# Kernel tuning notes

Hardware: AMD Instinct MI355X
Metric: run time of the kernel (lower is better)

The kernel has to match this reference:

```python
import jax, jax.numpy as jnp
import numpy as np
from jax import lax

DIM = 192
HEADS = 4
EPS = 1e-12  # torch F.normalize eps


def setup_inputs() -> dict:
    key = jax.random.key(0)
    k1, k2, k3, k4 = jax.random.split(key, 4)
    b, c, h, w = 8, DIM, 128, 128
    x = jax.random.normal(k1, (b, c, h, w), dtype=jnp.float32)
    w_qkv = jax.random.normal(k2, (3 * c, c), dtype=jnp.float32) * (1.0 / np.sqrt(c))
    w_dw = jax.random.normal(k3, (3 * c, 1, 3, 3), dtype=jnp.float32) * (1.0 / 3.0)
    temperature = jnp.ones((HEADS, 1, 1), dtype=jnp.float32)
    w_proj = jax.random.normal(k4, (c, c), dtype=jnp.float32) * (1.0 / np.sqrt(c))
    return {"x": x, "w_qkv": w_qkv, "w_dw": w_dw, "temperature": temperature, "w_proj": w_proj}


def _l2norm(t):
    # torch F.normalize(dim=-1): t / max(||t||_2, eps)
    n = jnp.sqrt(jnp.sum(t * t, axis=-1, keepdims=True))
    return t / jnp.maximum(n, EPS)


def reference(x, w_qkv, w_dw, temperature, w_proj):
    b, c, h, w = x.shape
    heads = HEADS
    hc = c // heads  # channels per head
    # 1x1 conv: dim -> 3*dim
    qkv = jnp.einsum('bchw,oc->bohw', x, w_qkv)
    # depthwise 3x3 conv, padding=1, no relu/norm
    qkv = lax.conv_general_dilated(
        qkv, w_dw, window_strides=(1, 1), padding='SAME',
        feature_group_count=3 * c,
        dimension_numbers=('NCHW', 'OIHW', 'NCHW'))
    q, k, v = jnp.split(qkv, 3, axis=1)
    # b (head c) h w -> b head c (h w)
    n = h * w
    q = q.reshape(b, heads, hc, n)
    k = k.reshape(b, heads, hc, n)
    v = v.reshape(b, heads, hc, n)
    q = _l2norm(q)
    k = _l2norm(k)
    # channel attention: [b, head, hc, hc]
    attn = jnp.einsum('bhcn,bhdn->bhcd', q, k) * temperature[None]
    attn = jax.nn.softmax(attn, axis=-1)
    out = jnp.einsum('bhcd,bhdn->bhcn', attn, v)
    out = out.reshape(b, c, h, w)
    out = jnp.einsum('bchw,oc->bohw', out, w_proj)
    return out
```

## Files before the change

kernel.cpp:

```cpp
#include <hip/hip_runtime.h>
#include <stdint.h>


typedef __attribute__((ext_vector_type(8))) short bf16x8;
typedef __attribute__((ext_vector_type(4))) float f32x4;
typedef unsigned short u16;

#define HW 16384
#define CD 192
#define O3 576
#define KD 192

__device__ __forceinline__ float b2f(u16 u) {
    union { unsigned int i; float f; } v; v.i = ((unsigned int)u) << 16; return v.f;
}
__device__ __forceinline__ u16 f2b(float f) {
    union { float f; unsigned int i; } v; v.f = f;
    return (u16)((v.i + 0x7fffu + ((v.i >> 16) & 1u)) >> 16);
}

__global__ __launch_bounds__(256) void fill_f32(float* p, long long n, float val) {
    long long stride = (long long)gridDim.x * 256;
    for (long long i = blockIdx.x * 256LL + threadIdx.x; i < n; i += stride) p[i] = val;
}

__global__ __launch_bounds__(256) void zerof(float* p, int n) {
    int i = blockIdx.x * 256 + threadIdx.x;
    if (i < n) p[i] = 0.f;
}

__global__ __launch_bounds__(256) void cvt_f2b(const float* __restrict__ in,
                                               u16* __restrict__ out, int n) {
    int i = blockIdx.x * 256 + threadIdx.x;
    if (i < n) out[i] = f2b(in[i]);
}

__global__ __launch_bounds__(256) void transpose_f2b(
    const float* __restrict__ in, u16* __restrict__ out,
    long long in_bs, long long out_bs)
{
    __shared__ u16 t[64 * 72];
    const int tid = threadIdx.x;
    const int p0 = blockIdx.x * 64, c0 = blockIdx.y * 64;
    const long long bz = blockIdx.z;
    const float* ib = in + bz * in_bs;
    u16* ob = out + bz * out_bs;
    {
        int cl = tid >> 2, pc = (tid & 3) * 16;
        const float* src = &ib[(long long)(c0 + cl) * HW + p0 + pc];
#pragma unroll
        for (int j4 = 0; j4 < 4; j4++) {
            f32x4 v = *(const f32x4*)(src + j4 * 4);
            u16* d = &t[cl * 72 + pc + j4 * 4];
            d[0] = f2b(v[0]); d[1] = f2b(v[1]); d[2] = f2b(v[2]); d[3] = f2b(v[3]);
        }
    }
    __syncthreads();
    {
        int pl = tid >> 2, cc = (tid & 3) * 16;
        u16 tmp[16] __attribute__((aligned(16)));
#pragma unroll
        for (int j = 0; j < 16; j++) tmp[j] = t[(cc + j) * 72 + pl];
        u16* dst = &ob[(long long)(p0 + pl) * CD + c0 + cc];
        *(bf16x8*)dst       = *(const bf16x8*)&tmp[0];
        *(bf16x8*)(dst + 8) = *(const bf16x8*)&tmp[8];
    }
}

__global__ __launch_bounds__(256) void transpose_b(
    const u16* __restrict__ in, u16* __restrict__ out,
    long long in_bs, long long out_bs)
{
    __shared__ u16 t[64 * 72];
    const int tid = threadIdx.x;
    const int p0 = blockIdx.x * 64, c0 = blockIdx.y * 64;
    const long long bz = blockIdx.z;
    const u16* ib = in + bz * in_bs;
    u16* ob = out + bz * out_bs;
    {
        int cl = tid >> 2, pc = (tid & 3) * 16;
        const u16* src = &ib[(long long)(c0 + cl) * HW + p0 + pc];
        *(bf16x8*)&t[cl * 72 + pc]     = *(const bf16x8*)src;
        *(bf16x8*)&t[cl * 72 + pc + 8] = *(const bf16x8*)(src + 8);
    }
    __syncthreads();
    {
        int pl = tid >> 2, cc = (tid & 3) * 16;
        u16 tmp[16] __attribute__((aligned(16)));
#pragma unroll
        for (int j = 0; j < 16; j++) tmp[j] = t[(cc + j) * 72 + pl];
        u16* dst = &ob[(long long)(p0 + pl) * CD + c0 + cc];
        *(bf16x8*)dst       = *(const bf16x8*)&tmp[0];
        *(bf16x8*)(dst + 8) = *(const bf16x8*)&tmp[8];
    }
}

__device__ __forceinline__ void stage16(const u16* g, u16* l) {
    __builtin_amdgcn_global_load_lds((const __attribute__((address_space(1))) unsigned int*)g,
                                     (__attribute__((address_space(3))) unsigned int*)l, 16, 0, 0);
}

template <bool OUT_F32>
__global__ __launch_bounds__(256) void gemm_bt(
    const u16* __restrict__ A, const u16* __restrict__ Bt, void* __restrict__ Cv,
    int M, long long a_bs, long long b_bs, long long c_bs)
{
    __shared__ u16 lsA[128 * 32];
    __shared__ u16 lsB[128 * 32];
    const int tid = threadIdx.x;
    const int lane = tid & 63, wid = tid >> 6;
    const int n0 = blockIdx.x * 128, m0 = blockIdx.y * 128;
    const long long bz = blockIdx.z;
    const u16* Ab = A + bz * a_bs;
    const u16* Bb = Bt + bz * b_bs;
    const int wm = (wid & 1) * 64, wn = (wid >> 1) * 64;
    const int lr = lane & 15, quad = lane >> 4;
    const int srow = lane >> 2, skc = (lane & 3) * 8;

    f32x4 acc[4][4];
#pragma unroll
    for (int i = 0; i < 4; i++)
#pragma unroll
        for (int j = 0; j < 4; j++) acc[i][j] = (f32x4){0.f, 0.f, 0.f, 0.f};

    for (int k0 = 0; k0 < KD; k0 += 32) {
        __syncthreads();
#pragma unroll
        for (int i = 0; i < 2; i++) {
            int ra = m0 + wid * 32 + i * 16 + srow;
            ra = ra < M ? ra : M - 1;
            stage16(Ab + (long long)ra * KD + k0 + skc, &lsA[(wid * 32 + i * 16) * 32]);
            int rb = n0 + wid * 32 + i * 16 + srow;
            stage16(Bb + (long long)rb * KD + k0 + skc, &lsB[(wid * 32 + i * 16) * 32]);
        }
        __syncthreads();
        bf16x8 af[4], bfv[4];
#pragma unroll
        for (int t = 0; t < 4; t++) {
            af[t]  = *(const bf16x8*)&lsA[(wm + t * 16 + lr) * 32 + quad * 8];
            bfv[t] = *(const bf16x8*)&lsB[(wn + t * 16 + lr) * 32 + quad * 8];
        }
#pragma unroll
        for (int mt = 0; mt < 4; mt++)
#pragma unroll
            for (int nt = 0; nt < 4; nt++)
                acc[mt][nt] = __builtin_amdgcn_mfma_f32_16x16x32_bf16(af[mt], bfv[nt], acc[mt][nt], 0, 0, 0);
    }
#pragma unroll
    for (int mt = 0; mt < 4; mt++)
#pragma unroll
        for (int r = 0; r < 4; r++) {
            int row = m0 + wm + mt * 16 + quad * 4 + r;
            if (row < M) {
#pragma unroll
                for (int nt = 0; nt < 4; nt++) {
                    int col = n0 + wn + nt * 16 + lr;
                    if (OUT_F32)
                        ((float*)Cv)[bz * c_bs + (long long)row * HW + col] = acc[mt][nt][r];
                    else
                        ((u16*)Cv)[bz * c_bs + (long long)row * HW + col] = f2b(acc[mt][nt][r]);
                }
            }
        }
}

__global__ __launch_bounds__(256) void dwconv2(
    const u16* __restrict__ in, const float* __restrict__ wdw, u16* __restrict__ outp,
    long long in_bs, long long out_bs, int wch0)
{
    const int rt = blockIdx.x, ch = blockIdx.y, tid = threadIdx.x;
    const long long bz = blockIdx.z;
    const u16* ip = in + bz * in_bs + (long long)ch * HW;
    u16* op = outp + bz * out_bs + (long long)ch * HW;
    __shared__ float t[18 * 132];
    const int r0 = rt * 16;
    if (tid < 18) {
        t[tid * 132 + 0] = 0.f;   t[tid * 132 + 129] = 0.f;
        t[tid * 132 + 130] = 0.f; t[tid * 132 + 131] = 0.f;
    }
    for (int i = tid; i < 288; i += 256) {
        int rr = i >> 4, cc = (i & 15) * 8;
        int gr = r0 + rr - 1;
        float f[8];
        if (gr >= 0 && gr < 128) {
            bf16x8 v = *(const bf16x8*)(ip + gr * 128 + cc);
#pragma unroll
            for (int j = 0; j < 8; j++) f[j] = b2f((u16)v[j]);
        } else {
#pragma unroll
            for (int j = 0; j < 8; j++) f[j] = 0.f;
        }
#pragma unroll
        for (int j = 0; j < 8; j++) t[rr * 132 + 1 + cc + j] = f[j];
    }
    float w[9];
#pragma unroll
    for (int j = 0; j < 9; j++) w[j] = wdw[(wch0 + ch) * 9 + j];
    __syncthreads();
    const int rr = tid >> 4, c8 = (tid & 15) * 8;
    float o[8] = {0.f, 0.f, 0.f, 0.f, 0.f, 0.f, 0.f, 0.f};
#pragma unroll
    for (int dy = 0; dy < 3; dy++) {
        const float* row = &t[(rr + dy) * 132 + c8];
        float r[12] __attribute__((aligned(16)));
        *(f32x4*)&r[0] = *(const f32x4*)row;
        *(f32x4*)&r[4] = *(const f32x4*)(row + 4);
        *(f32x4*)&r[8] = *(const f32x4*)(row + 8);
        const float w0 = w[dy * 3], w1 = w[dy * 3 + 1], w2 = w[dy * 3 + 2];
#pragma unroll
        for (int j = 0; j < 8; j++) o[j] += w0 * r[j] + w1 * r[j + 1] + w2 * r[j + 2];
    }
    u16 ob[8] __attribute__((aligned(16)));
#pragma unroll
    for (int j = 0; j < 8; j++) ob[j] = f2b(o[j]);
    *(bf16x8*)&op[(long long)(r0 + rr) * 128 + c8] = *(const bf16x8*)ob;
}

__global__ __launch_bounds__(256) void attn_scores(
    const u16* __restrict__ qk, float* __restrict__ S, float* __restrict__ norms,
    int bh0)
{
    const int tid = threadIdx.x, lane = tid & 63, wid = tid >> 6;
    const int kc = blockIdx.x, head = blockIdx.y;
    const long long bz = blockIdx.z;
    const u16* q = qk + bz * (2LL * CD * HW) + (long long)head * 48 * HW;
    const u16* k = q + (long long)CD * HW;
    const int lr = lane & 15, quad = lane >> 4;

    f32x4 sc[3][3], sq[3], sk[3];
#pragma unroll
    for (int i = 0; i < 3; i++) {
#pragma unroll
        for (int j = 0; j < 3; j++) sc[i][j] = (f32x4){0.f, 0.f, 0.f, 0.f};
        sq[i] = (f32x4){0.f, 0.f, 0.f, 0.f};
        sk[i] = (f32x4){0.f, 0.f, 0.f, 0.f};
    }
    const int n0 = kc * 1024 + wid * 256;
#pragma unroll 2
    for (int s = 0; s < 8; s++) {
        const int n = n0 + s * 32 + quad * 8;
        bf16x8 aq[3], ak[3];
#pragma unroll
        for (int t3 = 0; t3 < 3; t3++) {
            aq[t3] = *(const bf16x8*)(q + (long long)(t3 * 16 + lr) * HW + n);
            ak[t3] = *(const bf16x8*)(k + (long long)(t3 * 16 + lr) * HW + n);
        }
#pragma unroll
        for (int mt = 0; mt < 3; mt++)
#pragma unroll
            for (int nt = 0; nt < 3; nt++)
                sc[mt][nt] = __builtin_amdgcn_mfma_f32_16x16x32_bf16(aq[mt], ak[nt], sc[mt][nt], 0, 0, 0);
#pragma unroll
        for (int t3 = 0; t3 < 3; t3++) {
            sq[t3] = __builtin_amdgcn_mfma_f32_16x16x32_bf16(aq[t3], aq[t3], sq[t3], 0, 0, 0);
            sk[t3] = __builtin_amdgcn_mfma_f32_16x16x32_bf16(ak[t3], ak[t3], sk[t3], 0, 0, 0);
        }
    }
    __shared__ float sS[2304];
    __shared__ float snq[48], snk[48];
    for (int i = tid; i < 2304; i += 256) sS[i] = 0.f;
    if (tid < 48) { snq[tid] = 0.f; snk[tid] = 0.f; }
    __syncthreads();
#pragma unroll
    for (int mt = 0; mt < 3; mt++)
#pragma unroll
        for (int nt = 0; nt < 3; nt++)
#pragma unroll
            for (int r = 0; r < 4; r++)
                atomicAdd(&sS[(mt * 16 + quad * 4 + r) * 48 + nt * 16 + lr], sc[mt][nt][r]);
#pragma unroll
    for (int t3 = 0; t3 < 3; t3++)
#pragma unroll
        for (int r = 0; r < 4; r++) {
            int rw = quad * 4 + r;
            if (rw == lr) {
                atomicAdd(&snq[t3 * 16 + rw], sq[t3][r]);
                atomicAdd(&snk[t3 * 16 + rw], sk[t3][r]);
            }
        }
    __syncthreads();
    const int bh = bh0 + (int)bz * 4 + head;
    float* Sg = S + (long long)bh * 2304;
    for (int i = tid; i < 2304; i += 256) atomicAdd(&Sg[i], sS[i]);
    float* ng = norms + bh * 96;
    if (tid < 48) atomicAdd(&ng[tid], snq[tid]);
    else if (tid < 96) atomicAdd(&ng[tid], snk[tid - 48]);
}

__global__ __launch_bounds__(64) void softmax_k(
    const float* __restrict__ S, const float* __restrict__ norms,
    const float* __restrict__ temp, float* __restrict__ attn, int bh0)
{
    const int bh = bh0 + blockIdx.x, head = bh & 3, r = threadIdx.x;
    if (r >= 48) return;
    const float tv = temp[head];
    const float* Sg = S + (long long)bh * 2304;
    const float* ng = norms + bh * 96;
    const float nq = fmaxf(sqrtf(ng[r]), 1e-12f);
    float lg[48];
    float mx = -1e30f;
#pragma unroll
    for (int d = 0; d < 48; d++) {
        float nk = fmaxf(sqrtf(ng[48 + d]), 1e-12f);
        float v = Sg[r * 48 + d] * tv / (nq * nk);
        lg[d] = v; mx = fmaxf(mx, v);
    }
    float sum = 0.f;
#pragma unroll
    for (int d = 0; d < 48; d++) { float e = __expf(lg[d] - mx); lg[d] = e; sum += e; }
    const float inv = 1.f / sum;
    float* Ag = attn + (long long)bh * 2304 + r * 48;
#pragma unroll
    for (int d = 0; d < 48; d++) Ag[d] = lg[d] * inv;
}

__global__ __launch_bounds__(256) void mproj(
    const float* __restrict__ wproj, const float* __restrict__ attn, u16* __restrict__ Mm,
    int b0)
{
    const int ob = blockIdx.x, b = b0 + blockIdx.y, tid = threadIdx.x;
    __shared__ float sA[9216];
    const float* Ab = attn + (long long)b * 9216;
    for (int i = tid; i < 9216; i += 256) sA[i] = Ab[i];
    __syncthreads();
    for (int i = tid; i < 48 * 192; i += 256) {
        int o = ob * 48 + i / 192;
        int cc = i % 192;
        int h = cc / 48, d = cc - h * 48;
        const float* wr = wproj + o * 192 + h * 48;
        const float* ar = &sA[h * 2304 + d];
        float acc = 0.f;
        for (int c = 0; c < 48; c++) acc += wr[c] * ar[c * 48];
        Mm[(long long)b * 36864 + o * 192 + cc] = f2b(acc);
    }
}

extern "C" void kernel_launch(void* const* d_in, const int* in_sizes, int n_in,
                              void* d_out, int out_size, void* d_ws, size_t ws_size,
                              hipStream_t stream)
{
    const float* x     = (const float*)d_in[0];
    const float* wqkv  = (const float*)d_in[1];
    const float* wdw   = (const float*)d_in[2];
    const float* temp  = (const float*)d_in[3];
    const float* wproj = (const float*)d_in[4];
    float* out = (float*)d_out;
    char* ws = (char*)d_ws;
    const long long CHW = (long long)CD * HW;

    if (ws_size < 2097152ULL + 31457280ULL) {
        fill_f32<<<2048, 256, 0, stream>>>(out, out_size, 100.0f);
        return;
    }
    int G = 8;
    while (G > 1 && (unsigned long long)(2097152ULL + (unsigned long long)G * 31457280ULL) > (unsigned long long)ws_size)
        G >>= 1;

    float* S      = (float*)ws;
    float* norms  = (float*)(ws + 294912);
    float* attn   = (float*)(ws + 307200);
    u16*   Mm     = (u16*)(ws + 602112);
    u16*   wqkv_b = (u16*)(ws + 1191936);
    u16* region1  = (u16*)(ws + 2097152);
    u16* qkv_pre  = region1 + (long long)G * 2 * CHW;

    zerof<<<300, 256, 0, stream>>>(S, 76800);
    cvt_f2b<<<432, 256, 0, stream>>>(wqkv, wqkv_b, O3 * KD);

    for (int g0 = 0; g0 < 8; g0 += G) {
        transpose_f2b<<<dim3(256, 3, G), 256, 0, stream>>>(
            x + (long long)g0 * CHW, region1, CHW, CHW);
        gemm_bt<false><<<dim3(128, 5, G), 256, 0, stream>>>(
            wqkv_b, region1, qkv_pre, O3, 0LL, CHW, 3LL * CHW);
        dwconv2<<<dim3(8, 384, G), 256, 0, stream>>>(
            qkv_pre, wdw, region1, 3LL * CHW, 2LL * CHW, 0);
        dwconv2<<<dim3(8, 192, G), 256, 0, stream>>>(
            qkv_pre + 2LL * CHW, wdw, qkv_pre, 3LL * CHW, 3LL * CHW, 384);
        attn_scores<<<dim3(16, 4, G), 256, 0, stream>>>(region1, S, norms, g0 * 4);
        softmax_k<<<4 * G, 64, 0, stream>>>(S, norms, temp, attn, g0 * 4);
        mproj<<<dim3(4, G), 256, 0, stream>>>(wproj, attn, Mm, g0);
        transpose_b<<<dim3(256, 3, G), 256, 0, stream>>>(
            qkv_pre, qkv_pre + CHW, 3LL * CHW, 3LL * CHW);
        gemm_bt<true><<<dim3(128, 2, G), 256, 0, stream>>>(
            Mm + (long long)g0 * 36864, qkv_pre + CHW, out + (long long)g0 * CHW,
            CD, 36864LL, 3LL * CHW, CHW);
    }
}
```

Measured before the change: 433.5 us.

## Prepack A operands into MFMA fragment layout and stage full-K B tile once

The weight matrices (wqkv and the per-batch projection matrix) are pre-arranged into MFMA register fragment order, so each wave loads its A fragments straight from global memory into registers without LDS staging. The B tile for the whole K=192 dimension is staged into LDS once with an XOR swizzle, removing the per-k-step sync loop and bank conflicts. This raises register and LDS use per block, with occupancy pinned to 2 blocks via launch bounds, and mproj now writes its output in the fragment layout.

```diff
diff --git a/kernel.cpp b/kernel.cpp
--- a/kernel.cpp
+++ b/kernel.cpp
@@ -29,10 +29,25 @@
     if (i < n) p[i] = 0.f;
 }
 
-__global__ __launch_bounds__(256) void cvt_f2b(const float* __restrict__ in,
-                                               u16* __restrict__ out, int n) {
-    int i = blockIdx.x * 256 + threadIdx.x;
-    if (i < n) out[i] = f2b(in[i]);
+__global__ __launch_bounds__(256) void afrag_prep(
+    const float* __restrict__ W, u16* __restrict__ Af, int M, int NF)
+{
+    int t = blockIdx.x * 256 + threadIdx.x;
+    if (t >= NF * 64) return;
+    int F = t >> 6, lane = t & 63;
+    int ks = F % 6, mt = (F / 6) & 3, rwmb = F / 24;
+    int row = rwmb * 64 + mt * 16 + (lane & 15);
+    int k0 = ks * 32 + (lane >> 4) * 8;
+    u16 v[8] __attribute__((aligned(16)));
+    if (row < M) {
+        const float* src = W + (long long)row * KD + k0;
+#pragma unroll
+        for (int j = 0; j < 8; j++) v[j] = f2b(src[j]);
+    } else {
+#pragma unroll
+        for (int j = 0; j < 8; j++) v[j] = 0;
+    }
+    *(bf16x8*)&Af[(long long)F * 512 + lane * 8] = *(const bf16x8*)v;
 }
 
 __global__ __launch_bounds__(256) void transpose_f2b(
@@ -101,51 +116,61 @@
 }
 
 template <bool OUT_F32>
-__global__ __launch_bounds__(256) void gemm_bt(
-    const u16* __restrict__ A, const u16* __restrict__ Bt, void* __restrict__ Cv,
-    int M, long long a_bs, long long b_bs, long long c_bs)
-{
-    __shared__ u16 lsA[128 * 32];
-    __shared__ u16 lsB[128 * 32];
+__global__ __launch_bounds__(256, 2) void gemm_af(
+    const u16* __restrict__ Afrag, const u16* __restrict__ Bt, void* __restrict__ Cv,
+    int M, long long af_bs, long long b_bs, long long c_bs)
+{
+    __shared__ u16 lsB[6][128 * 32];
     const int tid = threadIdx.x;
     const int lane = tid & 63, wid = tid >> 6;
-    const int n0 = blockIdx.x * 128, m0 = blockIdx.y * 128;
+    const int n0 = blockIdx.x * 128, mb = blockIdx.y;
     const long long bz = blockIdx.z;
-    const u16* Ab = A + bz * a_bs;
     const u16* Bb = Bt + bz * b_bs;
     const int wm = (wid & 1) * 64, wn = (wid >> 1) * 64;
     const int lr = lane & 15, quad = lane >> 4;
-    const int srow = lane >> 2, skc = (lane & 3) * 8;
-
+
+    {
+        const int srow = lane >> 2;
+        const int gslot = (lane & 3) ^ (srow & 3);
+        const u16* gp = Bb + (long long)(n0 + wid * 32 + srow) * KD + gslot * 8;
+#pragma unroll
+        for (int ks = 0; ks < 6; ks++) {
+            stage16(gp + ks * 32,               &lsB[ks][(wid * 32) * 32]);
+            stage16(gp + 16 * KD + ks * 32,     &lsB[ks][(wid * 32 + 16) * 32]);
+        }
+    }
+    bf16x8 af[4][6];
+    {
+        const u16* Ap = Afrag + bz * af_bs
+                      + ((long long)((mb * 2 + (wid & 1)) * 24)) * 512 + lane * 8;
+#pragma unroll
+        for (int mt = 0; mt < 4; mt++)
+#pragma unroll
+            for (int ks = 0; ks < 6; ks++)
+                af[mt][ks] = *(const bf16x8*)(Ap + (mt * 6 + ks) * 512);
+    }
     f32x4 acc[4][4];
 #pragma unroll
     for (int i = 0; i < 4; i++)
 #pragma unroll
         for (int j = 0; j < 4; j++) acc[i][j] = (f32x4){0.f, 0.f, 0.f, 0.f};
 
-    for (int k0 = 0; k0 < KD; k0 += 32) {
-        __syncthreads();
-#pragma unroll
-        for (int i = 0; i < 2; i++) {
-            int ra = m0 + wid * 32 + i * 16 + srow;
-            ra = ra < M ? ra : M - 1;
-            stage16(Ab + (long long)ra * KD + k0 + skc, &lsA[(wid * 32 + i * 16) * 32]);
-            int rb = n0 + wid * 32 + i * 16 + srow;
-            stage16(Bb + (long long)rb * KD + k0 + skc, &lsB[(wid * 32 + i * 16) * 32]);
-        }
-        __syncthreads();
-        bf16x8 af[4], bfv[4];
-#pragma unroll
-        for (int t = 0; t < 4; t++) {
-            af[t]  = *(const bf16x8*)&lsA[(wm + t * 16 + lr) * 32 + quad * 8];
-            bfv[t] = *(const bf16x8*)&lsB[(wn + t * 16 + lr) * 32 + quad * 8];
-        }
+    __syncthreads();
+
+    const int rslot = (quad ^ (lr & 3)) * 8;
+#pragma unroll
+    for (int ks = 0; ks < 6; ks++) {
+        bf16x8 bfv[4];
+#pragma unroll
+        for (int nt = 0; nt < 4; nt++)
+            bfv[nt] = *(const bf16x8*)&lsB[ks][(wn + nt * 16 + lr) * 32 + rslot];
 #pragma unroll
         for (int mt = 0; mt < 4; mt++)
 #pragma unroll
             for (int nt = 0; nt < 4; nt++)
-                acc[mt][nt] = __builtin_amdgcn_mfma_f32_16x16x32_bf16(af[mt], bfv[nt], acc[mt][nt], 0, 0, 0);
-    }
+                acc[mt][nt] = __builtin_amdgcn_mfma_f32_16x16x32_bf16(af[mt][ks], bfv[nt], acc[mt][nt], 0, 0, 0);
+    }
+    const int m0 = mb * 128;
 #pragma unroll
     for (int mt = 0; mt < 4; mt++)
 #pragma unroll
@@ -331,7 +356,9 @@
         const float* ar = &sA[h * 2304 + d];
         float acc = 0.f;
         for (int c = 0; c < 48; c++) acc += wr[c] * ar[c * 48];
-        Mm[(long long)b * 36864 + o * 192 + cc] = f2b(acc);
+        int fi = (o >> 6) * 24 + ((o >> 4) & 3) * 6 + (cc >> 5);
+        int lanei = ((cc >> 3) & 3) * 16 + (o & 15);
+        Mm[(long long)b * 49152 + (long long)fi * 512 + lanei * 8 + (cc & 7)] = f2b(acc);
     }
 }
 
@@ -359,30 +386,30 @@
     float* S      = (float*)ws;
     float* norms  = (float*)(ws + 294912);
     float* attn   = (float*)(ws + 307200);
-    u16*   Mm     = (u16*)(ws + 602112);
-    u16*   wqkv_b = (u16*)(ws + 1191936);
+    u16*   MmF    = (u16*)(ws + 602112);
+    u16*   wqkvF  = (u16*)(ws + 1388544);
     u16* region1  = (u16*)(ws + 2097152);
     u16* qkv_pre  = region1 + (long long)G * 2 * CHW;
 
     zerof<<<300, 256, 0, stream>>>(S, 76800);
-    cvt_f2b<<<432, 256, 0, stream>>>(wqkv, wqkv_b, O3 * KD);
+    afrag_prep<<<60, 256, 0, stream>>>(wqkv, wqkvF, O3, 240);
 
     for (int g0 = 0; g0 < 8; g0 += G) {
         transpose_f2b<<<dim3(256, 3, G), 256, 0, stream>>>(
             x + (long long)g0 * CHW, region1, CHW, CHW);
-        gemm_bt<false><<<dim3(128, 5, G), 256, 0, stream>>>(
-            wqkv_b, region1, qkv_pre, O3, 0LL, CHW, 3LL * CHW);
+        gemm_af<false><<<dim3(128, 5, G), 256, 0, stream>>>(
+            wqkvF, region1, qkv_pre, O3, 0LL, CHW, 3LL * CHW);
         dwconv2<<<dim3(8, 384, G), 256, 0, stream>>>(
             qkv_pre, wdw, region1, 3LL * CHW, 2LL * CHW, 0);
         dwconv2<<<dim3(8, 192, G), 256, 0, stream>>>(
             qkv_pre + 2LL * CHW, wdw, qkv_pre, 3LL * CHW, 3LL * CHW, 384);
         attn_scores<<<dim3(16, 4, G), 256, 0, stream>>>(region1, S, norms, g0 * 4);
         softmax_k<<<4 * G, 64, 0, stream>>>(S, norms, temp, attn, g0 * 4);
-        mproj<<<dim3(4, G), 256, 0, stream>>>(wproj, attn, Mm, g0);
+        mproj<<<dim3(4, G), 256, 0, stream>>>(wproj, attn, MmF, g0);
         transpose_b<<<dim3(256, 3, G), 256, 0, stream>>>(
             qkv_pre, qkv_pre + CHW, 3LL * CHW, 3LL * CHW);
-        gemm_bt<true><<<dim3(128, 2, G), 256, 0, stream>>>(
-            Mm + (long long)g0 * 36864, qkv_pre + CHW, out + (long long)g0 * CHW,
-            CD, 36864LL, 3LL * CHW, CHW);
-    }
-}
+        gemm_af<true><<<dim3(128, 2, G), 256, 0, stream>>>(
+            MmF + (long long)g0 * 49152, qkv_pre + CHW, out + (long long)g0 * CHW,
+            CD, 49152LL, 3LL * CHW, CHW);
+    }
+}
```

New measurement: 436.2 us. About the same (+0.6%).
